# Kernel optimization log

Hardware: AMD Instinct MI355X
Metric: run time of the kernel (lower is better)

Reference implementation:

```python
import jax, jax.numpy as jnp
import numpy as np


def _temporal_gated_conv(x, W, b):
    """x: (B,T,N,C) -> (B,T-Kt+1,N,Co). W: (1,Kt,C,2*Co), b: (2*Co,).
    Matches torch Conv2d(in,2*out,(1,Kt)) over (B,C,N,T) followed by GLU."""
    xh = x.transpose(0, 2, 1, 3)  # (B,N,T,C) as NHWC, kernel (1,Kt) over (N,T)
    y = jax.lax.conv_general_dilated(
        xh, W, window_strides=(1, 1), padding='VALID',
        dimension_numbers=('NHWC', 'HWIO', 'NHWC')) + b  # (B,N,T',2Co)
    lhs, rhs = jnp.split(y, 2, axis=-1)
    y = lhs * jax.nn.sigmoid(rhs)
    return y.transpose(0, 2, 1, 3)  # (B,T',N,Co)


def _spatial_graph_conv(x, cheb, Theta):
    """x: (B,T,N,C), cheb: (K,N,N), Theta: (K,C,Co).
    Faithful to torch code: step_x is CUMULATIVELY multiplied by T_k."""
    K = cheb.shape[0]
    cur = x
    acc = jnp.zeros(x.shape[:3] + (Theta.shape[-1],), dtype=x.dtype)
    for k in range(K):  # K is small and structural
        cur = jnp.einsum('mn,btnc->btmc', cheb[k], cur)
        acc = acc + jnp.einsum('btnc,co->btno', cur, Theta[k])
    return jax.nn.relu(acc)


def setup_inputs() -> dict:
    key = jax.random.key(0)
    ks = jax.random.split(key, 7)
    B, T, N, C = 16, 64, 1024, 2
    Kt, Kc, temporal_dim, spatial_dim = 3, 3, 64, 16
    s = 0.05
    return {
        'x': jax.random.normal(ks[0], (B, T, N, C), jnp.float32),
        'cheb': jax.random.normal(ks[1], (Kc, N, N), jnp.float32) * (1.0 / np.sqrt(N)),
        'W1': jax.random.normal(ks[2], (1, Kt, C, 2 * temporal_dim), jnp.float32) * s,
        'b1': jax.random.normal(ks[3], (2 * temporal_dim,), jnp.float32) * s,
        'Theta': jax.random.normal(ks[4], (Kc, temporal_dim, spatial_dim), jnp.float32) * s,
        'W2': jax.random.normal(ks[5], (1, Kt, spatial_dim, 2 * temporal_dim), jnp.float32) * s,
        'b2': jax.random.normal(ks[6], (2 * temporal_dim,), jnp.float32) * s,
    }


def reference(x, cheb, W1, b1, Theta, W2, b2):
    h = _temporal_gated_conv(x, W1, b1)          # (B, T-Kt+1, N, temporal_dim)
    h = _spatial_graph_conv(h, cheb, Theta)      # (B, T-Kt+1, N, spatial_dim)
    out = _temporal_gated_conv(h, W2, b2)        # (B, T-2*(Kt-1), N, temporal_dim)
    return out
```

## Files before the change

kernel.cpp:

```cpp
#include <hip/hip_runtime.h>
#include <stdint.h>

typedef __attribute__((ext_vector_type(8))) short bf16x8;
typedef __attribute__((ext_vector_type(4))) float f32x4;

__device__ __forceinline__ unsigned short f2bf(float f) {
  union { float f; unsigned u; } v; v.f = f;
  unsigned r = v.u + 0x7FFFu + ((v.u >> 16) & 1u);
  return (unsigned short)(r >> 16);
}

__device__ __forceinline__ float sigm(float x) { return 1.0f / (1.0f + __expf(-x)); }

__device__ __forceinline__ void gload16(const void* g, void* l) {
  __builtin_amdgcn_global_load_lds((const __attribute__((address_space(1))) void*)g,
                                   (__attribute__((address_space(3))) void*)l, 16, 0, 0);
}

__device__ __forceinline__ void bar() {
  __builtin_amdgcn_sched_barrier(0);
  __builtin_amdgcn_s_barrier();
  __builtin_amdgcn_sched_barrier(0);
}

__global__ void k0_prep(const float* __restrict__ cheb, unsigned short* __restrict__ cb1,
                        unsigned short* __restrict__ cb2, unsigned short* __restrict__ Pbig) {
  int i = blockIdx.x * blockDim.x + threadIdx.x;
  unsigned short h = f2bf(cheb[i]);
  int which = i >> 20, r = i & 1048575;
  if (which == 0) Pbig[(size_t)(r >> 10) * 3072 + (r & 1023)] = h;
  else if (which == 1) cb1[r] = h;
  else cb2[r] = h;
}

__global__ void tposebf(const unsigned short* __restrict__ s1, int ss1, unsigned short* __restrict__ d1,
                        const unsigned short* __restrict__ s2, int ss2, unsigned short* __restrict__ d2) {
  const unsigned short* src = blockIdx.z ? s2 : s1;
  unsigned short* dst = blockIdx.z ? d2 : d1;
  const int ss = blockIdx.z ? ss2 : ss1;
  __shared__ unsigned short t[64][65];
  const int c = threadIdx.x & 63, r4 = threadIdx.x >> 6;
  const int r0 = blockIdx.y * 64, c0 = blockIdx.x * 64;
#pragma unroll
  for (int r = 0; r < 64; r += 4) t[r + r4][c] = src[(size_t)(r0 + r + r4) * ss + c0 + c];
  __syncthreads();
#pragma unroll
  for (int r = 0; r < 64; r += 4) dst[(size_t)(c0 + r + r4) * 1024 + r0 + c] = t[c][r + r4];
}

__global__ __launch_bounds__(256) void gemm_bt(
    const unsigned short* __restrict__ A, const unsigned short* __restrict__ Bt,
    unsigned short* __restrict__ C, int K, int ldc, int coloff,
    const unsigned short* __restrict__ A2, const unsigned short* __restrict__ Bt2,
    unsigned short* __restrict__ C2, int ldc2, int coloff2) {
  __shared__ __align__(16) unsigned short sA[128 * 32];
  __shared__ __align__(16) unsigned short sB[128 * 32];
  const unsigned short* Ap = A;
  const unsigned short* Bp = Bt;
  unsigned short* Cp = C;
  int ld = ldc, co = coloff;
  if (blockIdx.z) { Ap = A2; Bp = Bt2; Cp = C2; ld = ldc2; co = coloff2; }
  const int mb = blockIdx.x, nb = blockIdx.y;
  const int tid = threadIdx.x;
  const int lane = tid & 63;
  const int w = tid >> 6;
  const int m0 = mb * 128, n0 = nb * 128;
  const int wm = (w >> 1) * 64, wn = (w & 1) * 64;
  const int lr = lane & 15, lg = lane >> 4;
  const f32x4 ZV = {0.f, 0.f, 0.f, 0.f};
  f32x4 acc[4][4];
#pragma unroll
  for (int f = 0; f < 4; ++f)
#pragma unroll
    for (int g = 0; g < 4; ++g) acc[f][g] = ZV;
  const int r2 = tid >> 2, kp = tid & 3;
  const size_t rowA0 = (size_t)(m0 + r2) * K;
  const size_t rowA1 = (size_t)(m0 + 64 + r2) * K;
  const size_t rowB0 = (size_t)(n0 + r2) * K;
  const size_t rowB1 = (size_t)(n0 + 64 + r2) * K;
  unsigned short* la = &sA[w * 512];
  unsigned short* lb = &sB[w * 512];
  for (int k0 = 0; k0 < K; k0 += 32) {
    const int kc = k0 + kp * 8;
    gload16(Ap + rowA0 + kc, la);
    gload16(Ap + rowA1 + kc, la + 2048);
    gload16(Bp + rowB0 + kc, lb);
    gload16(Bp + rowB1 + kc, lb + 2048);
    __syncthreads();
    bf16x8 av[4], bv[4];
#pragma unroll
    for (int f = 0; f < 4; ++f)
      av[f] = *(const bf16x8*)&sA[(wm + f * 16 + lr) * 32 + lg * 8];
#pragma unroll
    for (int g = 0; g < 4; ++g)
      bv[g] = *(const bf16x8*)&sB[(wn + g * 16 + lr) * 32 + lg * 8];
#pragma unroll
    for (int f = 0; f < 4; ++f)
#pragma unroll
      for (int g = 0; g < 4; ++g)
        acc[f][g] = __builtin_amdgcn_mfma_f32_16x16x32_bf16(av[f], bv[g], acc[f][g], 0, 0, 0);
    __syncthreads();
  }
#pragma unroll
  for (int f = 0; f < 4; ++f) {
    const int m = m0 + wm + f * 16 + lg * 4;
#pragma unroll
    for (int g = 0; g < 4; ++g) {
      const int col = co + n0 + wn + g * 16 + lr;
#pragma unroll
      for (int i = 0; i < 4; ++i)
        Cp[(size_t)(m + i) * ld + col] = f2bf(acc[f][g][i]);
    }
  }
}

__device__ __forceinline__ void dec_chunk(int s, int& row, int& c) {
  const int r3 = (((s >> 2) ^ (s >> 4)) & 1) | (((s >> 3) & 1) << 1) | (((s >> 4) & 1) << 2);
  const int u = s ^ r3;
  row = u >> 2;
  c = u & 3;
}

__global__ __launch_bounds__(512, 2) void gemm_big(
    const unsigned short* __restrict__ A, const unsigned short* __restrict__ Bt,
    unsigned short* __restrict__ C) {
  constexpr int K = 3072, NT = 96;
  __shared__ __align__(16) unsigned short lds[4 * 16384];
  const int tid = threadIdx.x;
  const int lane = tid & 63, w = tid >> 6;
  const int wr = w >> 2, wc = w & 3;
  const int lr = lane & 15, lg = lane >> 4;
  const int lin = blockIdx.x;
  const int v = (lin & 7) * 31 + (lin >> 3);
  const int mb = v & 3, nb = v >> 2;
  const int m0 = mb * 256, n0 = nb * 256;

  int r0_, c0_, r1_, c1_;
  dec_chunk((w * 2 + 0) * 64 + lane, r0_, c0_);
  dec_chunk((w * 2 + 1) * 64 + lane, r1_, c1_);
  const unsigned short* sA0 = A + (size_t)(m0 + r0_) * K + c0_ * 8;
  const unsigned short* sA1 = A + (size_t)(m0 + r1_) * K + c1_ * 8;
  const unsigned short* sB0 = Bt + (size_t)(n0 + r0_) * K + c0_ * 8;
  const unsigned short* sB1 = Bt + (size_t)(n0 + r1_) * K + c1_ * 8;
  const int ldsoff0 = (w * 2 + 0) * 512, ldsoff1 = (w * 2 + 1) * 512;

  f32x4 acc[8][4];
  const f32x4 ZV = {0.f, 0.f, 0.f, 0.f};
#pragma unroll
  for (int f = 0; f < 8; ++f)
#pragma unroll
    for (int g = 0; g < 4; ++g) acc[f][g] = ZV;

  const int aoff = (((wr * 128 + lr) * 64 + lg * 16) ^ ((lr & 7) << 4));
  const int boff = (((wc * 64 + lr) * 64 + lg * 16) ^ ((lr & 7) << 4));

  bf16x8 avA[8], bvA[4], avB[8], bvB[4];

#define STAGE(T)                                               \
  do {                                                         \
    unsigned short* ba_ = lds + ((T) & 3) * 16384;             \
    const int k0_ = (T) * 32;                                  \
    gload16(sA0 + k0_, ba_ + ldsoff0);                         \
    gload16(sA1 + k0_, ba_ + ldsoff1);                         \
    gload16(sB0 + k0_, ba_ + 8192 + ldsoff0);                  \
    gload16(sB1 + k0_, ba_ + 8192 + ldsoff1);                  \
  } while (0)

#define DSREAD(T, AN, BN)                                      \
  do {                                                         \
    const char* rb_ = (const char*)lds + ((T) & 3) * 32768;    \
    _Pragma("unroll") for (int f_ = 0; f_ < 8; ++f_)           \
      AN[f_] = *(const bf16x8*)(rb_ + aoff + f_ * 1024);       \
    _Pragma("unroll") for (int g_ = 0; g_ < 4; ++g_)           \
      BN[g_] = *(const bf16x8*)(rb_ + 16384 + boff + g_ * 1024); \
  } while (0)

#define MFMAC(AC, BC)                                          \
  do {                                                         \
    __builtin_amdgcn_s_setprio(1);                             \
    _Pragma("unroll") for (int f_ = 0; f_ < 8; ++f_)           \
      _Pragma("unroll") for (int g_ = 0; g_ < 4; ++g_)         \
        acc[f_][g_] = __builtin_amdgcn_mfma_f32_16x16x32_bf16(AC[f_], BC[g_], acc[f_][g_], 0, 0, 0); \
    __builtin_amdgcn_s_setprio(0);                             \
  } while (0)

  STAGE(0); STAGE(1); STAGE(2); STAGE(3);
  asm volatile("s_waitcnt vmcnt(8)" ::: "memory");
  bar();
  DSREAD(0, avA, bvA);

  for (int tt = 0; tt < NT - 4; tt += 2) {
    DSREAD(tt + 1, avB, bvB);
    STAGE(tt + 4);
    MFMAC(avA, bvA);
    asm volatile("s_waitcnt vmcnt(8) lgkmcnt(0)" ::: "memory");
    bar();
    DSREAD(tt + 2, avA, bvA);
    STAGE(tt + 5);
    MFMAC(avB, bvB);
    asm volatile("s_waitcnt vmcnt(8) lgkmcnt(0)" ::: "memory");
    bar();
  }
  DSREAD(93, avB, bvB);
  MFMAC(avA, bvA);
  asm volatile("s_waitcnt vmcnt(4) lgkmcnt(0)" ::: "memory");
  bar();
  DSREAD(94, avA, bvA);
  MFMAC(avB, bvB);
  asm volatile("s_waitcnt vmcnt(0) lgkmcnt(0)" ::: "memory");
  bar();
  DSREAD(95, avB, bvB);
  MFMAC(avA, bvA);
  asm volatile("s_waitcnt lgkmcnt(0)" ::: "memory");
  __builtin_amdgcn_sched_barrier(0);
  MFMAC(avB, bvB);
#undef STAGE
#undef DSREAD
#undef MFMAC

#pragma unroll
  for (int g = 0; g < 4; ++g) {
    const int n = n0 + wc * 64 + g * 16;
    const size_t jb = (size_t)(n >> 4) * 16384;
#pragma unroll
    for (int f = 0; f < 8; ++f) {
      const int m = m0 + wr * 128 + f * 16 + lg * 4;
#pragma unroll
      for (int i = 0; i < 4; ++i)
        C[jb + (size_t)(m + i) * 16 + lr] = f2bf(fmaxf(acc[f][g][i], 0.f));
    }
  }
}

__global__ __launch_bounds__(256) void k1_fused(
    const float* __restrict__ x, const float* __restrict__ W1, const float* __restrict__ b1,
    const float* __restrict__ Theta, unsigned short* __restrict__ Zt) {
  __shared__ __align__(16) unsigned short hs[4 * 64 * 68];
  __shared__ __align__(16) unsigned short th[3 * 16 * 72];
  __shared__ __align__(16) unsigned short tr[64 * 68];
  const int tid = threadIdx.x, lane = tid & 63, w = tid >> 6;
  const int n0 = blockIdx.x * 64;
  const int bt0 = blockIdx.y * 4;
  const int bt = bt0 + w;
  const int b = bt / 62, t = bt - b * 62;
  float xv[6];
#pragma unroll
  for (int kt = 0; kt < 3; ++kt) {
    const float2 p = *(const float2*)&x[(size_t)((b * 64 + t + kt) * 1024 + n0 + lane) * 2];
    xv[kt * 2] = p.x;
    xv[kt * 2 + 1] = p.y;
  }
  float h[64];
#pragma unroll
  for (int ch = 0; ch < 64; ++ch) {
    float l = b1[ch], r = b1[64 + ch];
#pragma unroll
    for (int q = 0; q < 6; ++q) {
      l += xv[q] * W1[q * 128 + ch];
      r += xv[q] * W1[q * 128 + 64 + ch];
    }
    h[ch] = l * sigm(r);
  }
#pragma unroll
  for (int c8 = 0; c8 < 8; ++c8) {
    union { unsigned short u[8]; uint4 v; } pk;
#pragma unroll
    for (int j = 0; j < 8; ++j) pk.u[j] = f2bf(h[c8 * 8 + j]);
    *(uint4*)&hs[(w * 64 + lane) * 68 + c8 * 8] = pk.v;
  }
  for (int idx = tid; idx < 3072; idx += 256) {
    const int kc = idx >> 10, o = (idx >> 6) & 15, c = idx & 63;
    th[kc * 1152 + o * 72 + c] = f2bf(Theta[((kc << 6) | c) * 16 + o]);
  }
  __syncthreads();
  const int lr = lane & 15, lg = lane >> 4;
  const f32x4 ZV = {0.f, 0.f, 0.f, 0.f};
  for (int kc = 0; kc < 3; ++kc) {
    const bf16x8 av0 = *(const bf16x8*)&th[kc * 1152 + lr * 72 + lg * 8];
    const bf16x8 av1 = *(const bf16x8*)&th[kc * 1152 + lr * 72 + 32 + lg * 8];
    f32x4 acc[4];
#pragma unroll
    for (int ns = 0; ns < 4; ++ns) acc[ns] = ZV;
#pragma unroll
    for (int ns = 0; ns < 4; ++ns) {
      const bf16x8 bv0 = *(const bf16x8*)&hs[(w * 64 + ns * 16 + lr) * 68 + lg * 8];
      const bf16x8 bv1 = *(const bf16x8*)&hs[(w * 64 + ns * 16 + lr) * 68 + 32 + lg * 8];
      acc[ns] = __builtin_amdgcn_mfma_f32_16x16x32_bf16(av0, bv0, acc[ns], 0, 0, 0);
      acc[ns] = __builtin_amdgcn_mfma_f32_16x16x32_bf16(av1, bv1, acc[ns], 0, 0, 0);
    }
    if (kc) __syncthreads();
#pragma unroll
    for (int ns = 0; ns < 4; ++ns)
#pragma unroll
      for (int i = 0; i < 4; ++i)
        tr[(w * 16 + lg * 4 + i) * 68 + ns * 16 + lr] = f2bf(acc[ns][i]);
    __syncthreads();
#pragma unroll
    for (int rd = 0; rd < 2; ++rd) {
      const int cidx = rd * 256 + tid;
      const int rl = cidx >> 3, ck = cidx & 7;
      const uint4 v = *(const uint4*)&tr[rl * 68 + ck * 8];
      *(uint4*)&Zt[(size_t)(bt0 * 16 + rl) * 3072 + kc * 1024 + n0 + ck * 8] = v;
    }
  }
}

__global__ __launch_bounds__(256) void k3_out(
    const unsigned short* __restrict__ accb, const float* __restrict__ W2,
    const float* __restrict__ b2, float* __restrict__ out) {
  __shared__ __align__(16) unsigned short sW[128 * 72];
  const int tid = threadIdx.x, lane = tid & 63, w = tid >> 6;
  const int lr = lane & 15, lg = lane >> 4;
  const int n0 = blockIdx.x * 256;
  const int btp = blockIdx.y;
  const int b = btp / 60, tt = btp - b * 60;
  for (int idx = tid; idx < 2048; idx += 256) {
    const int ch = idx >> 4, k = 48 + (idx & 15);
    sW[ch * 72 + k] = 0;
  }
  for (int idx = tid; idx < 6144; idx += 256) {
    const int k = idx >> 7, ch = idx & 127;
    sW[ch * 72 + k] = f2bf(W2[idx]);
  }
  const int rowb = n0 + w * 64;
  const bf16x8 ZB = {0, 0, 0, 0, 0, 0, 0, 0};
  bf16x8 av[4][2];
#pragma unroll
  for (int f = 0; f < 4; ++f)
#pragma unroll
    for (int hh = 0; hh < 2; ++hh) {
      const int gk = hh * 32 + lg * 8;
      const int kt = gk >> 4, ci = gk & 15;
      av[f][hh] = ZB;
      if (kt < 3)
        av[f][hh] = *(const bf16x8*)&accb[(size_t)(b * 62 + tt + kt) * 16384 +
                                          (size_t)(rowb + f * 16 + lr) * 16 + ci];
    }
  __syncthreads();
  const size_t obase = (size_t)(b * 60 + tt) * 65536;
  const f32x4 ZV = {0.f, 0.f, 0.f, 0.f};
#pragma unroll
  for (int gl = 0; gl < 4; ++gl) {
    const int chl = gl * 16 + lr;
    const bf16x8 bl0 = *(const bf16x8*)&sW[chl * 72 + lg * 8];
    const bf16x8 bl1 = *(const bf16x8*)&sW[chl * 72 + 32 + lg * 8];
    const bf16x8 br0 = *(const bf16x8*)&sW[(64 + chl) * 72 + lg * 8];
    const bf16x8 br1 = *(const bf16x8*)&sW[(64 + chl) * 72 + 32 + lg * 8];
    f32x4 aL[4], aR[4];
#pragma unroll
    for (int f = 0; f < 4; ++f) { aL[f] = ZV; aR[f] = ZV; }
#pragma unroll
    for (int f = 0; f < 4; ++f) {
      aL[f] = __builtin_amdgcn_mfma_f32_16x16x32_bf16(av[f][0], bl0, aL[f], 0, 0, 0);
      aL[f] = __builtin_amdgcn_mfma_f32_16x16x32_bf16(av[f][1], bl1, aL[f], 0, 0, 0);
      aR[f] = __builtin_amdgcn_mfma_f32_16x16x32_bf16(av[f][0], br0, aR[f], 0, 0, 0);
      aR[f] = __builtin_amdgcn_mfma_f32_16x16x32_bf16(av[f][1], br1, aR[f], 0, 0, 0);
    }
    const float bbl = b2[chl], bbr = b2[64 + chl];
#pragma unroll
    for (int f = 0; f < 4; ++f)
#pragma unroll
      for (int i = 0; i < 4; ++i) {
        const float pl = aL[f][i] + bbl;
        const float pr = aR[f][i] + bbr;
        out[obase + (size_t)(rowb + f * 16 + lg * 4 + i) * 64 + chl] = pl * sigm(pr);
      }
  }
}

extern "C" void kernel_launch(void* const* d_in, const int* in_sizes, int n_in,
                              void* d_out, int out_size, void* d_ws, size_t ws_size,
                              hipStream_t stream) {
  const float* x    = (const float*)d_in[0];
  const float* cheb = (const float*)d_in[1];
  const float* W1   = (const float*)d_in[2];
  const float* b1   = (const float*)d_in[3];
  const float* Th   = (const float*)d_in[4];
  const float* W2   = (const float*)d_in[5];
  const float* b2   = (const float*)d_in[6];
  float* out = (float*)d_out;

  char* ws = (char*)d_ws;
  const size_t MB = 1u << 20;
  unsigned short* cb1  = (unsigned short*)(ws);
  unsigned short* cb2  = (unsigned short*)(ws + 2 * MB);
  unsigned short* Pbig = (unsigned short*)(ws + 4 * MB);
  unsigned short* t0   = (unsigned short*)(ws + 10 * MB);
  unsigned short* t1   = (unsigned short*)(ws + 12 * MB);
  unsigned short* Qb   = (unsigned short*)(ws + 14 * MB);
  unsigned short* accb = (unsigned short*)(ws + 14 * MB);
  unsigned short* Zt   = (unsigned short*)d_out;

  k0_prep<<<12288, 256, 0, stream>>>(cheb, cb1, cb2, Pbig);
  tposebf<<<dim3(16, 16, 2), 256, 0, stream>>>(Pbig, 3072, t0, cb1, 1024, t1);
  gemm_bt<<<dim3(8, 8, 2), 256, 0, stream>>>(cb1, t0, Pbig, 1024, 3072, 1024,
                                             cb2, t1, Qb, 1024, 0);
  gemm_bt<<<dim3(8, 8, 1), 256, 0, stream>>>(Qb, t0, Pbig, 1024, 3072, 2048,
                                             cb1, t0, Pbig, 1024, 0);
  k1_fused<<<dim3(16, 248), 256, 0, stream>>>(x, W1, b1, Th, Zt);
  gemm_big<<<dim3(248), dim3(512), 0, stream>>>(Pbig, Zt, accb);
  k3_out<<<dim3(4, 960), 256, 0, stream>>>(accb, W2, b2, out);
}
```

Before: 296.9 us.

## Split-K the Chebyshev product GEMMs and fuse the prep and transpose kernels

Merges the bf16 conversion of cheb and the transposes into one kernel. The two 1024^3 cheb-product GEMMs now split K four ways into fp32 partial buffers, with a separate reduce kernel that sums the partials, converts to bf16 and writes into Pbig/Qb. This raises the block count from 64/128 to 256/512 to fill more CUs on these small GEMMs. The cost is extra fp32 partial traffic and two more launches.

After: 286.0 us. 3.7% less time.

```diff
diff --git a/kernel.cpp b/kernel.cpp
--- a/kernel.cpp
+++ b/kernel.cpp
@@ -23,44 +23,42 @@
   __builtin_amdgcn_sched_barrier(0);
 }
 
-__global__ void k0_prep(const float* __restrict__ cheb, unsigned short* __restrict__ cb1,
-                        unsigned short* __restrict__ cb2, unsigned short* __restrict__ Pbig) {
-  int i = blockIdx.x * blockDim.x + threadIdx.x;
-  unsigned short h = f2bf(cheb[i]);
-  int which = i >> 20, r = i & 1048575;
-  if (which == 0) Pbig[(size_t)(r >> 10) * 3072 + (r & 1023)] = h;
-  else if (which == 1) cb1[r] = h;
-  else cb2[r] = h;
-}
-
-__global__ void tposebf(const unsigned short* __restrict__ s1, int ss1, unsigned short* __restrict__ d1,
-                        const unsigned short* __restrict__ s2, int ss2, unsigned short* __restrict__ d2) {
-  const unsigned short* src = blockIdx.z ? s2 : s1;
-  unsigned short* dst = blockIdx.z ? d2 : d1;
-  const int ss = blockIdx.z ? ss2 : ss1;
+__global__ void k0t(const float* __restrict__ cheb, unsigned short* __restrict__ cb1,
+                    unsigned short* __restrict__ cb2, unsigned short* __restrict__ Pbig,
+                    unsigned short* __restrict__ t0, unsigned short* __restrict__ t1) {
   __shared__ unsigned short t[64][65];
+  const int z = blockIdx.z;
   const int c = threadIdx.x & 63, r4 = threadIdx.x >> 6;
   const int r0 = blockIdx.y * 64, c0 = blockIdx.x * 64;
-#pragma unroll
-  for (int r = 0; r < 64; r += 4) t[r + r4][c] = src[(size_t)(r0 + r + r4) * ss + c0 + c];
+  const float* src = cheb + (size_t)z * 1048576;
+#pragma unroll
+  for (int r = 0; r < 64; r += 4) {
+    const int rr = r0 + r + r4;
+    const unsigned short h = f2bf(src[(size_t)rr * 1024 + c0 + c]);
+    t[r + r4][c] = h;
+    if (z == 0) Pbig[(size_t)rr * 3072 + c0 + c] = h;
+    else if (z == 1) cb1[(size_t)rr * 1024 + c0 + c] = h;
+    else cb2[(size_t)rr * 1024 + c0 + c] = h;
+  }
   __syncthreads();
-#pragma unroll
-  for (int r = 0; r < 64; r += 4) dst[(size_t)(c0 + r + r4) * 1024 + r0 + c] = t[c][r + r4];
-}
-
-__global__ __launch_bounds__(256) void gemm_bt(
-    const unsigned short* __restrict__ A, const unsigned short* __restrict__ Bt,
-    unsigned short* __restrict__ C, int K, int ldc, int coloff,
-    const unsigned short* __restrict__ A2, const unsigned short* __restrict__ Bt2,
-    unsigned short* __restrict__ C2, int ldc2, int coloff2) {
+  if (z == 2) return;
+  unsigned short* dst = z ? t1 : t0;
+#pragma unroll
+  for (int r = 0; r < 64; r += 4)
+    dst[(size_t)(c0 + r + r4) * 1024 + r0 + c] = t[c][r + r4];
+}
+
+__global__ __launch_bounds__(256) void gemm_splitk(
+    const unsigned short* __restrict__ A1, const unsigned short* __restrict__ B1,
+    float* __restrict__ C1,
+    const unsigned short* __restrict__ A2, const unsigned short* __restrict__ B2,
+    float* __restrict__ C2) {
   __shared__ __align__(16) unsigned short sA[128 * 32];
   __shared__ __align__(16) unsigned short sB[128 * 32];
-  const unsigned short* Ap = A;
-  const unsigned short* Bp = Bt;
-  unsigned short* Cp = C;
-  int ld = ldc, co = coloff;
-  if (blockIdx.z) { Ap = A2; Bp = Bt2; Cp = C2; ld = ldc2; co = coloff2; }
-  const int mb = blockIdx.x, nb = blockIdx.y;
+  const unsigned short* Ap = blockIdx.z ? A2 : A1;
+  const unsigned short* Bp = blockIdx.z ? B2 : B1;
+  float* Cp = blockIdx.z ? C2 : C1;
+  const int mb = blockIdx.x & 7, nb = blockIdx.x >> 3, ks = blockIdx.y;
   const int tid = threadIdx.x;
   const int lane = tid & 63;
   const int w = tid >> 6;
@@ -74,13 +72,14 @@
 #pragma unroll
     for (int g = 0; g < 4; ++g) acc[f][g] = ZV;
   const int r2 = tid >> 2, kp = tid & 3;
-  const size_t rowA0 = (size_t)(m0 + r2) * K;
-  const size_t rowA1 = (size_t)(m0 + 64 + r2) * K;
-  const size_t rowB0 = (size_t)(n0 + r2) * K;
-  const size_t rowB1 = (size_t)(n0 + 64 + r2) * K;
+  const size_t rowA0 = (size_t)(m0 + r2) * 1024;
+  const size_t rowA1 = (size_t)(m0 + 64 + r2) * 1024;
+  const size_t rowB0 = (size_t)(n0 + r2) * 1024;
+  const size_t rowB1 = (size_t)(n0 + 64 + r2) * 1024;
   unsigned short* la = &sA[w * 512];
   unsigned short* lb = &sB[w * 512];
-  for (int k0 = 0; k0 < K; k0 += 32) {
+  const int kbase = ks * 256;
+  for (int k0 = kbase; k0 < kbase + 256; k0 += 32) {
     const int kc = k0 + kp * 8;
     gload16(Ap + rowA0 + kc, la);
     gload16(Ap + rowA1 + kc, la + 2048);
@@ -101,17 +100,38 @@
         acc[f][g] = __builtin_amdgcn_mfma_f32_16x16x32_bf16(av[f], bv[g], acc[f][g], 0, 0, 0);
     __syncthreads();
   }
+  float* Cb = Cp + (size_t)ks * 1048576;
 #pragma unroll
   for (int f = 0; f < 4; ++f) {
     const int m = m0 + wm + f * 16 + lg * 4;
 #pragma unroll
     for (int g = 0; g < 4; ++g) {
-      const int col = co + n0 + wn + g * 16 + lr;
+      const int col = n0 + wn + g * 16 + lr;
 #pragma unroll
       for (int i = 0; i < 4; ++i)
-        Cp[(size_t)(m + i) * ld + col] = f2bf(acc[f][g][i]);
-    }
-  }
+        Cb[(size_t)(m + i) * 1024 + col] = acc[f][g][i];
+    }
+  }
+}
+
+__global__ void reducep(const float* __restrict__ S1, unsigned short* __restrict__ D1, int ld1, int co1,
+                        const float* __restrict__ S2, unsigned short* __restrict__ D2, int ld2, int co2) {
+  const float* S = blockIdx.z ? S2 : S1;
+  unsigned short* D = blockIdx.z ? D2 : D1;
+  const int ld = blockIdx.z ? ld2 : ld1;
+  const int co = blockIdx.z ? co2 : co1;
+  const int e = (blockIdx.x * 256 + threadIdx.x) * 4;
+  const float4 a = *(const float4*)&S[e];
+  const float4 b = *(const float4*)&S[1048576 + e];
+  const float4 c = *(const float4*)&S[2097152 + e];
+  const float4 d = *(const float4*)&S[3145728 + e];
+  const int row = e >> 10, col = e & 1023;
+  ushort4 o;
+  o.x = f2bf(a.x + b.x + c.x + d.x);
+  o.y = f2bf(a.y + b.y + c.y + d.y);
+  o.z = f2bf(a.z + b.z + c.z + d.z);
+  o.w = f2bf(a.w + b.w + c.w + d.w);
+  *(ushort4*)&D[(size_t)row * ld + co + col] = o;
 }
 
 __device__ __forceinline__ void dec_chunk(int s, int& row, int& c) {
@@ -389,14 +409,16 @@
   unsigned short* t1   = (unsigned short*)(ws + 12 * MB);
   unsigned short* Qb   = (unsigned short*)(ws + 14 * MB);
   unsigned short* accb = (unsigned short*)(ws + 14 * MB);
+  float*          P1f  = (float*)(ws + 48 * MB);
+  float*          Qf   = (float*)(ws + 64 * MB);
+  float*          P2f  = (float*)(ws + 80 * MB);
   unsigned short* Zt   = (unsigned short*)d_out;
 
-  k0_prep<<<12288, 256, 0, stream>>>(cheb, cb1, cb2, Pbig);
-  tposebf<<<dim3(16, 16, 2), 256, 0, stream>>>(Pbig, 3072, t0, cb1, 1024, t1);
-  gemm_bt<<<dim3(8, 8, 2), 256, 0, stream>>>(cb1, t0, Pbig, 1024, 3072, 1024,
-                                             cb2, t1, Qb, 1024, 0);
-  gemm_bt<<<dim3(8, 8, 1), 256, 0, stream>>>(Qb, t0, Pbig, 1024, 3072, 2048,
-                                             cb1, t0, Pbig, 1024, 0);
+  k0t<<<dim3(16, 16, 3), 256, 0, stream>>>(cheb, cb1, cb2, Pbig, t0, t1);
+  gemm_splitk<<<dim3(64, 4, 2), 256, 0, stream>>>(cb1, t0, P1f, cb2, t1, Qf);
+  reducep<<<dim3(1024, 1, 2), 256, 0, stream>>>(P1f, Pbig, 3072, 1024, Qf, Qb, 1024, 0);
+  gemm_splitk<<<dim3(64, 4, 1), 256, 0, stream>>>(Qb, t0, P2f, Qb, t0, P2f);
+  reducep<<<dim3(1024, 1, 1), 256, 0, stream>>>(P2f, Pbig, 3072, 2048, P2f, Pbig, 3072, 2048);
   k1_fused<<<dim3(16, 248), 256, 0, stream>>>(x, W1, b1, Th, Zt);
   gemm_big<<<dim3(248), dim3(512), 0, stream>>>(Pbig, Zt, accb);
   k3_out<<<dim3(4, 960), 256, 0, stream>>>(accb, W2, b2, out);
```
